# Kernel tuning notes

Hardware: AMD Instinct MI355X
Metric: run time of the kernel (lower is better)

## Reference

```python
import jax, jax.numpy as jnp
import numpy as np

K = 3      # kernel_size
PAD = 1    # (dilation*(K-1)+1)//2 with dilation=1
EPS = 1e-3 # keras BatchNormalization default epsilon


def _unfold(x, k=K, pad=PAD):
    # reflect-pad local-window gather, torch.nn.functional.unfold ordering
    # x: [N,C,H,W] -> [N,C,k*k,H*W]
    N, C, H, W = x.shape
    xp = jnp.pad(x, ((0, 0), (0, 0), (pad, pad), (pad, pad)), mode='reflect')
    pats = jnp.stack([xp[:, :, i:i + H, j:j + W] for i in range(k) for j in range(k)], axis=2)
    return pats.reshape(N, C, k * k, H * W)


def _position(H, W):
    # [1,2,H,W]: channel 0 = x(-1..1 across W), channel 1 = y(-1..1 across H)
    loc_w = jnp.tile(jnp.linspace(-1.0, 1.0, W)[None, :], (H, 1))
    loc_h = jnp.tile(jnp.linspace(-1.0, 1.0, H)[:, None], (1, W))
    return jnp.stack([loc_w, loc_h], axis=0)[None].astype(jnp.float32)


def _bn(x, g, b, m, v):
    # keras BN, default axis=-1 (here the H*W axis), inference mode
    return (x - m) / jnp.sqrt(v + EPS) * g + b


def setup_inputs():
    key = jax.random.key(0)
    ks = jax.random.split(key, 16)
    N, C, H, W = 16, 256, 56, 56
    REL, OUT, SHARE = 16, 64, 8
    HW = H * W
    f = lambda k_, s: jax.random.normal(k_, s, dtype=jnp.float32)
    return {
        'x': f(ks[0], (N, C, H, W)),
        'conv1_w': f(ks[1], (REL, C)) * 0.05,
        'conv2_w': f(ks[2], (REL, C)) * 0.05,
        'conv3_w': f(ks[3], (OUT, C)) * 0.05,
        'convp_w': f(ks[4], (2, 2)),
        'convw1_w': f(ks[5], (REL, REL + 2)) * 0.2,
        'convw2_w': f(ks[6], (OUT // SHARE, REL)) * 0.2,
        'bn1_gamma': 1.0 + 0.1 * f(ks[7], (HW,)),
        'bn1_beta': 0.1 * f(ks[8], (HW,)),
        'bn1_mean': 0.1 * f(ks[9], (HW,)),
        'bn1_var': 1.0 + 0.5 * jax.random.uniform(ks[10], (HW,), dtype=jnp.float32),
        'bn2_gamma': 1.0 + 0.1 * f(ks[11], (HW,)),
        'bn2_beta': 0.1 * f(ks[12], (HW,)),
        'bn2_mean': 0.1 * f(ks[13], (HW,)),
        'bn2_var': 1.0 + 0.5 * jax.random.uniform(ks[14], (HW,), dtype=jnp.float32),
    }


def reference(x, conv1_w, conv2_w, conv3_w, convp_w, convw1_w, convw2_w,
              bn1_gamma, bn1_beta, bn1_mean, bn1_var,
              bn2_gamma, bn2_beta, bn2_mean, bn2_var):
    N, C, H, W = x.shape
    HW = H * W
    # 1x1 convs (channels_first) as channel contractions
    x1 = jnp.einsum('oc,nchw->nohw', conv1_w, x)
    x2 = jnp.einsum('oc,nchw->nohw', conv2_w, x)
    x3 = jnp.einsum('oc,nchw->nohw', conv3_w, x)
    p = jnp.einsum('oc,nchw->nohw', convp_w, _position(H, W))  # [1,2,H,W]
    # subtraction2(x1, x2): center feature minus windowed neighbors -> [N,rel,k^2,HW]
    sub2 = x1.reshape(N, -1, 1, HW) - _unfold(x2)
    # subtraction(p): relative positions -> [1,2,k^2,HW], tiled over batch
    subp = p.reshape(1, 2, 1, HW) - _unfold(p)
    rel = jnp.concatenate([sub2, jnp.tile(subp, (N, 1, 1, 1))], axis=1)  # [N,rel+2,k^2,HW]
    # conv_w: BN -> ReLU -> 1x1 conv -> BN -> ReLU -> 1x1 conv
    h = jax.nn.relu(_bn(rel, bn1_gamma, bn1_beta, bn1_mean, bn1_var))
    h = jnp.einsum('oc,ncjl->nojl', convw1_w, h)
    h = jax.nn.relu(_bn(h, bn2_gamma, bn2_beta, bn2_mean, bn2_var))
    h = jnp.einsum('oc,ncjl->nojl', convw2_w, h)  # [N,out//share,k^2,HW]
    w = jax.nn.softmax(h, axis=-2)                # softmax over the k^2 window axis
    # aggregation: weighted neighbor sum, weight channel shared by share_planes channels
    xu = _unfold(x3)                              # [N,out,k^2,HW]
    c_w = w.shape[1]
    xu = xu.reshape(N, -1, c_w, K * K, HW)        # channel c -> (c//c_w, c%c_w)
    out = jnp.einsum('ncjl,ngcjl->ngcl', w, xu)   # sum over window positions j
    return out.reshape(N, -1, H, W)
```

## Files before the change

kernel.cpp:

```cpp
#include <hip/hip_runtime.h>

typedef short bf16x8 __attribute__((ext_vector_type(8)));
typedef float floatx4 __attribute__((ext_vector_type(4)));
typedef unsigned short ushort4v __attribute__((ext_vector_type(4)));

#define HW 3136
#define NB 16

#define P_CP   0
#define P_W1   4
#define P_W2   292
#define P_FLAG 420
#define P_BN   424
#define PREP_FLOATS (424 + 4 * HW)

#define WS 100

__device__ __forceinline__ unsigned short f2bf(float f) {
    unsigned int u = __float_as_uint(f);
    unsigned int r = (u + 0x7FFFu + ((u >> 16) & 1u)) >> 16;
    return (unsigned short)r;
}
__device__ __forceinline__ float bf2f(unsigned short u) {
    return __uint_as_float(((unsigned int)u) << 16);
}
__device__ __forceinline__ void unp8(uint4 u, float* o) {
    o[0] = bf2f((unsigned short)(u.x & 0xFFFFu)); o[1] = bf2f((unsigned short)(u.x >> 16));
    o[2] = bf2f((unsigned short)(u.y & 0xFFFFu)); o[3] = bf2f((unsigned short)(u.y >> 16));
    o[4] = bf2f((unsigned short)(u.z & 0xFFFFu)); o[5] = bf2f((unsigned short)(u.z >> 16));
    o[6] = bf2f((unsigned short)(u.w & 0xFFFFu)); o[7] = bf2f((unsigned short)(u.w >> 16));
}
__device__ __forceinline__ float ldp(const void* p, int i, int isb) {
    return isb ? bf2f(((const unsigned short*)p)[i]) : ((const float*)p)[i];
}

__device__ __forceinline__ int detect_bf16(const void* varp, int* sflag) {
    if (threadIdx.x == 0) {
        const unsigned short* p = (const unsigned short*)varp;
        int ok = 1;
        for (int i = 0; i < 64; ++i) {
            unsigned short v = p[2 * i];
            if (v < 0x3F80u || v > 0x3FC0u) { ok = 0; break; }
        }
        *sflag = ok;
    }
    __syncthreads();
    return *sflag;
}

struct Stage { unsigned int b[8]; bf16x8 a[2]; };

__device__ __forceinline__ void load_stage(
    int isb, const void* x, size_t xbase, int cb,
    const void* const (&wsA)[2], const int (&roA)[2], int col, Stage& st)
{
    if (isb) {
        const unsigned short* xb = (const unsigned short*)x;
        #pragma unroll
        for (int j = 0; j < 8; ++j)
            st.b[j] = *(const unsigned int*)(xb + xbase + (size_t)(cb + j) * HW);
        #pragma unroll
        for (int rt = 0; rt < 2; ++rt)
            st.a[rt] = *(const bf16x8*)((const unsigned short*)wsA[rt] + (roA[rt] + col) * 256 + cb);
    } else {
        const float* xb = (const float*)x;
        #pragma unroll
        for (int j = 0; j < 8; ++j) {
            float2 f = *(const float2*)(xb + xbase + (size_t)(cb + j) * HW);
            st.b[j] = (unsigned int)f2bf(f.x) | ((unsigned int)f2bf(f.y) << 16);
        }
        #pragma unroll
        for (int rt = 0; rt < 2; ++rt) {
            const float* fp = (const float*)wsA[rt] + (roA[rt] + col) * 256 + cb;
            bf16x8 af;
            #pragma unroll
            for (int j = 0; j < 8; ++j) af[j] = (short)f2bf(fp[j]);
            st.a[rt] = af;
        }
    }
}

__global__ __launch_bounds__(384) void proj_kernel(
    const void* __restrict__ x,
    const void* __restrict__ w1, const void* __restrict__ w2,
    const void* __restrict__ w3,
    const void* __restrict__ cpw, const void* __restrict__ cw1,
    const void* __restrict__ cw2,
    const void* __restrict__ b1g, const void* __restrict__ b1b,
    const void* __restrict__ b1m, const void* __restrict__ b1v,
    const void* __restrict__ b2g, const void* __restrict__ b2b,
    const void* __restrict__ b2m, const void* __restrict__ b2v,
    unsigned short* __restrict__ y,
    float* __restrict__ prep)
{
    __shared__ int sflag;
    const int isb = detect_bf16(b1v, &sflag);
    const int tid = threadIdx.x;

    if (blockIdx.x == 0) {
        for (int i = tid; i < 4;   i += 384) prep[P_CP + i] = ldp(cpw, i, isb);
        for (int i = tid; i < 288; i += 384) prep[P_W1 + i] = ldp(cw1, i, isb);
        for (int i = tid; i < 128; i += 384) prep[P_W2 + i] = ldp(cw2, i, isb);
        if (tid == 0) prep[P_FLAG] = isb ? 1.f : 0.f;
        for (int i = tid; i < HW; i += 384) {
            float a1 = ldp(b1g, i, isb) * rsqrtf(ldp(b1v, i, isb) + 1e-3f);
            float c1 = ldp(b1b, i, isb) - ldp(b1m, i, isb) * a1;
            float a2 = ldp(b2g, i, isb) * rsqrtf(ldp(b2v, i, isb) + 1e-3f);
            float c2 = ldp(b2b, i, isb) - ldp(b2m, i, isb) * a2;
            prep[P_BN + i]          = a1;
            prep[P_BN + HW + i]     = c1;
            prep[P_BN + 2 * HW + i] = a2;
            prep[P_BN + 3 * HW + i] = c2;
        }
    }

    const int blk  = blockIdx.x;
    const int n    = blk / 49;
    const int wave = tid >> 6, lane = tid & 63;
    const int s    = wave & 1;
    const int rg   = wave >> 1;
    const int col  = lane & 15, quad = lane >> 4;
    const int lb   = (blk - n * 49) * 64 + s * 32;
    const int px   = lb + 2 * col;

    const void* wsA[2]; int roA[2];
    if (rg == 0)      { wsA[0] = w1; roA[0] = 0;  wsA[1] = w2; roA[1] = 0;  }
    else if (rg == 1) { wsA[0] = w3; roA[0] = 0;  wsA[1] = w3; roA[1] = 16; }
    else              { wsA[0] = w3; roA[0] = 32; wsA[1] = w3; roA[1] = 48; }

    const size_t xbase = (size_t)n * 256 * HW + px;

    floatx4 acc[2][2];
    const floatx4 z4 = {0.f, 0.f, 0.f, 0.f};
    #pragma unroll
    for (int rt = 0; rt < 2; ++rt)
        #pragma unroll
        for (int t = 0; t < 2; ++t) acc[rt][t] = z4;

    Stage st[2];
    load_stage(isb, x, xbase, quad * 8, wsA, roA, col, st[0]);
    #pragma unroll
    for (int q = 0; q < 8; ++q) {
        if (q < 7)
            load_stage(isb, x, xbase, (q + 1) * 32 + quad * 8, wsA, roA, col, st[(q + 1) & 1]);
        Stage& c = st[q & 1];
        bf16x8 bt0, bt1;
        #pragma unroll
        for (int j = 0; j < 8; ++j) {
            bt0[j] = (short)(c.b[j] & 0xFFFFu);
            bt1[j] = (short)(c.b[j] >> 16);
        }
        #pragma unroll
        for (int rt = 0; rt < 2; ++rt) {
            acc[rt][0] = __builtin_amdgcn_mfma_f32_16x16x32_bf16(c.a[rt], bt0, acc[rt][0], 0, 0, 0);
            acc[rt][1] = __builtin_amdgcn_mfma_f32_16x16x32_bf16(c.a[rt], bt1, acc[rt][1], 0, 0, 0);
        }
    }

    unsigned short* yb = y + ((size_t)n * HW + px) * 96 + rg * 32 + quad * 4;
    #pragma unroll
    for (int rt = 0; rt < 2; ++rt)
        #pragma unroll
        for (int t = 0; t < 2; ++t) {
            ushort4v pk;
            #pragma unroll
            for (int g = 0; g < 4; ++g) pk[g] = f2bf(acc[rt][t][g]);
            *(ushort4v*)(yb + (size_t)t * 96 + rt * 16) = pk;
        }
}

__global__ __launch_bounds__(576) void attn_kernel(
    const unsigned short* __restrict__ yT,
    const float* __restrict__ prep,
    void* __restrict__ out)
{
    __shared__ float wsm[64 * WS];
    const int tid = threadIdx.x;
    const int blk = blockIdx.x;
    const int n   = blk / 49;
    const int l0  = (blk - n * 49) * 64;
    const int isb = prep[P_FLAG] != 0.f;

    {
        const int j = tid >> 6;
        const int p = tid & 63;
        const int l = l0 + p;
        const int h = l / 56, w = l - h * 56;
        const int dy = j / 3 - 1, dx = j - (j / 3) * 3 - 1;
        int hh = h + dy; hh = (hh < 0) ? -hh : ((hh > 55) ? 110 - hh : hh);
        int ww = w + dx; ww = (ww < 0) ? -ww : ((ww > 55) ? 110 - ww : ww);
        const int nbr = hh * 56 + ww;

        const float a1 = prep[P_BN + l];
        const float c1 = prep[P_BN + HW + l];
        const float a2 = prep[P_BN + 2 * HW + l];
        const float c2 = prep[P_BN + 3 * HW + l];

        const unsigned short* y1p = yT + ((size_t)n * HW + l) * 96;
        const unsigned short* y2p = yT + ((size_t)n * HW + nbr) * 96 + 16;
        float y1f[16], y2f[16];
        unp8(*(const uint4*)y1p, y1f);       unp8(*(const uint4*)(y1p + 8), y1f + 8);
        unp8(*(const uint4*)y2p, y2f);       unp8(*(const uint4*)(y2p + 8), y2f + 8);

        float rel[18];
        #pragma unroll
        for (int c = 0; c < 16; ++c)
            rel[c] = fmaxf(fmaf(y1f[c] - y2f[c], a1, c1), 0.f);
        const float dlw = (float)(w - ww) * (2.0f / 55.0f);
        const float dlh = (float)(h - hh) * (2.0f / 55.0f);
        rel[16] = fmaxf(fmaf(prep[P_CP + 0] * dlw + prep[P_CP + 1] * dlh, a1, c1), 0.f);
        rel[17] = fmaxf(fmaf(prep[P_CP + 2] * dlw + prep[P_CP + 3] * dlh, a1, c1), 0.f);

        float h1[16];
        #pragma unroll
        for (int o = 0; o < 16; ++o) {
            float s = 0.f;
            #pragma unroll
            for (int c = 0; c < 18; ++c)
                s = fmaf(prep[P_W1 + o * 18 + c], rel[c], s);
            h1[o] = fmaxf(fmaf(s, a2, c2), 0.f);
        }
        float h2[8];
        #pragma unroll
        for (int o2 = 0; o2 < 8; ++o2) {
            float s = 0.f;
            #pragma unroll
            for (int o = 0; o < 16; ++o)
                s = fmaf(prep[P_W2 + o2 * 16 + o], h1[o], s);
            h2[o2] = s;
        }
        float* wp = &wsm[p * WS + j * 8];
        *(floatx4*)wp       = *(floatx4*)&h2[0];
        *(floatx4*)(wp + 4) = *(floatx4*)&h2[4];
    }
    __syncthreads();

    if (tid < 512) {
        const int c = tid & 7, p = tid >> 3;
        float v[9];
        #pragma unroll
        for (int j = 0; j < 9; ++j) v[j] = wsm[p * WS + j * 8 + c];
        float m = v[0];
        #pragma unroll
        for (int j = 1; j < 9; ++j) m = fmaxf(m, v[j]);
        float s = 0.f;
        #pragma unroll
        for (int j = 0; j < 9; ++j) { v[j] = __expf(v[j] - m); s += v[j]; }
        const float inv = 1.f / s;
        #pragma unroll
        for (int j = 0; j < 9; ++j) wsm[p * WS + j * 8 + c] = v[j] * inv;
    }
    __syncthreads();

    if (tid < 512) {
        const int p  = tid & 63;
        const int k8 = tid >> 6;
        const int l = l0 + p;
        const int h = l / 56, w = l - h * 56;
        int nbr[9];
        #pragma unroll
        for (int dy = 0; dy < 3; ++dy)
            #pragma unroll
            for (int dx = 0; dx < 3; ++dx) {
                int hh = h + dy - 1; hh = (hh < 0) ? -hh : ((hh > 55) ? 110 - hh : hh);
                int ww = w + dx - 1; ww = (ww < 0) ? -ww : ((ww > 55) ? 110 - ww : ww);
                nbr[dy * 3 + dx] = hh * 56 + ww;
            }
        const unsigned short* y3b = yT + (size_t)n * HW * 96 + 32 + k8 * 8;
        float acc8[8];
        #pragma unroll
        for (int k = 0; k < 8; ++k) acc8[k] = 0.f;
        #pragma unroll
        for (int j = 0; j < 9; ++j) {
            uint4 u = *(const uint4*)(y3b + (size_t)nbr[j] * 96);
            float yv[8];
            unp8(u, yv);
            const float* wp = &wsm[p * WS + j * 8];
            float2 w01 = *(const float2*)wp;
            float2 w23 = *(const float2*)(wp + 2);
            float2 w45 = *(const float2*)(wp + 4);
            float2 w67 = *(const float2*)(wp + 6);
            acc8[0] = fmaf(w01.x, yv[0], acc8[0]);
            acc8[1] = fmaf(w01.y, yv[1], acc8[1]);
            acc8[2] = fmaf(w23.x, yv[2], acc8[2]);
            acc8[3] = fmaf(w23.y, yv[3], acc8[3]);
            acc8[4] = fmaf(w45.x, yv[4], acc8[4]);
            acc8[5] = fmaf(w45.y, yv[5], acc8[5]);
            acc8[6] = fmaf(w67.x, yv[6], acc8[6]);
            acc8[7] = fmaf(w67.y, yv[7], acc8[7]);
        }
        const size_t obase = ((size_t)n * 64 + k8 * 8) * HW + l;
        #pragma unroll
        for (int k = 0; k < 8; ++k) {
            if (isb) ((unsigned short*)out)[obase + (size_t)k * HW] = f2bf(acc8[k]);
            else     ((float*)out)[obase + (size_t)k * HW]          = acc8[k];
        }
    }
}

extern "C" void kernel_launch(void* const* d_in, const int* in_sizes, int n_in,
                              void* d_out, int out_size, void* d_ws, size_t ws_size,
                              hipStream_t stream)
{
    const size_t yB = (size_t)NB * HW * 96 * 2;
    unsigned short* y = (unsigned short*)d_ws;
    float* prep = (float*)((char*)d_ws + yB);

    proj_kernel<<<dim3(784), dim3(384), 0, stream>>>(
        d_in[0], d_in[1], d_in[2], d_in[3],
        d_in[4], d_in[5], d_in[6],
        d_in[7], d_in[8], d_in[9], d_in[10],
        d_in[11], d_in[12], d_in[13], d_in[14],
        y, prep);

    attn_kernel<<<dim3(784), dim3(576), 0, stream>>>(y, prep, d_out);
}
```

Measured before the change: 165.6 us.

## Restructure projection GEMM with LDS-staged x tiles and move BN prep into attention kernel

The projection kernel becomes 128-thread blocks over 32 pixels. Each block stages the x tile in LDS using coalesced 16-byte loads, and every wave computes all six 16-row output tiles, so the B operand is reused across w1/w2/w3 instead of being reloaded per row group. It is templated on the input dtype so the branches disappear. The BN folding and the conv weight preparation move out of block 0 of the projection kernel into each attention block, which removes the global prep buffer and the serial work in block 0. The cost is redundant per-block BN and weight loads in the attention kernel, and extra __syncthreads in the projection k-loop.

```diff
diff --git a/kernel.cpp b/kernel.cpp
--- a/kernel.cpp
+++ b/kernel.cpp
@@ -3,17 +3,11 @@
 typedef short bf16x8 __attribute__((ext_vector_type(8)));
 typedef float floatx4 __attribute__((ext_vector_type(4)));
 typedef unsigned short ushort4v __attribute__((ext_vector_type(4)));
+typedef unsigned int uint4v __attribute__((ext_vector_type(4)));
 
 #define HW 3136
 #define NB 16
-
-#define P_CP   0
-#define P_W1   4
-#define P_W2   292
-#define P_FLAG 420
-#define P_BN   424
-#define PREP_FLOATS (424 + 4 * HW)
-
+#define LSTR 35
 #define WS 100
 
 __device__ __forceinline__ unsigned short f2bf(float f) {
@@ -48,138 +42,156 @@
     return *sflag;
 }
 
-struct Stage { unsigned int b[8]; bf16x8 a[2]; };
-
-__device__ __forceinline__ void load_stage(
-    int isb, const void* x, size_t xbase, int cb,
-    const void* const (&wsA)[2], const int (&roA)[2], int col, Stage& st)
-{
-    if (isb) {
-        const unsigned short* xb = (const unsigned short*)x;
-        #pragma unroll
-        for (int j = 0; j < 8; ++j)
-            st.b[j] = *(const unsigned int*)(xb + xbase + (size_t)(cb + j) * HW);
-        #pragma unroll
-        for (int rt = 0; rt < 2; ++rt)
-            st.a[rt] = *(const bf16x8*)((const unsigned short*)wsA[rt] + (roA[rt] + col) * 256 + cb);
+template <int ISB>
+__device__ __forceinline__ void stage_load(const void* x, size_t xrow, int kb,
+                                           int sc2, int spx, unsigned int (&o)[8])
+{
+    if (ISB) {
+        const unsigned short* p = (const unsigned short*)x + xrow + (size_t)(kb + 2 * sc2) * HW + spx;
+        uint4 e = *(const uint4*)p;
+        uint4 d = *(const uint4*)(p + HW);
+        o[0] = (e.x & 0xFFFFu) | (d.x << 16);
+        o[1] = (e.x >> 16)     | (d.x & 0xFFFF0000u);
+        o[2] = (e.y & 0xFFFFu) | (d.y << 16);
+        o[3] = (e.y >> 16)     | (d.y & 0xFFFF0000u);
+        o[4] = (e.z & 0xFFFFu) | (d.z << 16);
+        o[5] = (e.z >> 16)     | (d.z & 0xFFFF0000u);
+        o[6] = (e.w & 0xFFFFu) | (d.w << 16);
+        o[7] = (e.w >> 16)     | (d.w & 0xFFFF0000u);
     } else {
-        const float* xb = (const float*)x;
-        #pragma unroll
-        for (int j = 0; j < 8; ++j) {
-            float2 f = *(const float2*)(xb + xbase + (size_t)(cb + j) * HW);
-            st.b[j] = (unsigned int)f2bf(f.x) | ((unsigned int)f2bf(f.y) << 16);
-        }
-        #pragma unroll
-        for (int rt = 0; rt < 2; ++rt) {
-            const float* fp = (const float*)wsA[rt] + (roA[rt] + col) * 256 + cb;
-            bf16x8 af;
-            #pragma unroll
-            for (int j = 0; j < 8; ++j) af[j] = (short)f2bf(fp[j]);
-            st.a[rt] = af;
-        }
-    }
-}
-
-__global__ __launch_bounds__(384) void proj_kernel(
+        const float* p = (const float*)x + xrow + (size_t)(kb + 2 * sc2) * HW + spx;
+        floatx4 e0 = *(const floatx4*)p,        e1 = *(const floatx4*)(p + 4);
+        floatx4 d0 = *(const floatx4*)(p + HW), d1 = *(const floatx4*)(p + HW + 4);
+        #pragma unroll
+        for (int i = 0; i < 4; ++i) o[i]     = (unsigned int)f2bf(e0[i]) | ((unsigned int)f2bf(d0[i]) << 16);
+        #pragma unroll
+        for (int i = 0; i < 4; ++i) o[4 + i] = (unsigned int)f2bf(e1[i]) | ((unsigned int)f2bf(d1[i]) << 16);
+    }
+}
+
+template <int ISB>
+__device__ __forceinline__ bf16x8 loadA(const void* wp, int row, int cb)
+{
+    if (ISB) return *(const bf16x8*)((const unsigned short*)wp + row * 256 + cb);
+    const float* f = (const float*)wp + row * 256 + cb;
+    bf16x8 a;
+    #pragma unroll
+    for (int j = 0; j < 8; ++j) a[j] = (short)f2bf(f[j]);
+    return a;
+}
+
+template <int ISB>
+__device__ void proj_body(const void* x, const void* w1, const void* w2, const void* w3,
+                          unsigned int* buf, unsigned short* y,
+                          int n, int px0, int wv, int col, int quad, int sc2, int spx)
+{
+    const size_t xrow = (size_t)n * 256 * HW + px0;
+    const void* wp[6] = {w1, w2, w3, w3, w3, w3};
+    const int   ro[6] = {0, 0, 0, 16, 32, 48};
+
+    floatx4 acc[6] = {};
+    unsigned int st[8];
+    stage_load<ISB>(x, xrow, 0, sc2, spx, st);
+    #pragma unroll
+    for (int i = 0; i < 8; ++i) buf[(spx + i) * LSTR + sc2] = st[i];
+
+    bf16x8 Ac[6];
+    #pragma unroll
+    for (int r = 0; r < 6; ++r) Ac[r] = loadA<ISB>(wp[r], ro[r] + col, quad * 8);
+
+    const unsigned int* brow = &buf[(wv * 16 + col) * LSTR];
+
+    #pragma unroll
+    for (int ko = 0; ko < 4; ++ko) {
+        __syncthreads();
+        unsigned int nx[8];
+        if (ko < 3) stage_load<ISB>(x, xrow, 64 * (ko + 1), sc2, spx, nx);
+        #pragma unroll
+        for (int s = 0; s < 2; ++s) {
+            const int ss = ko * 2 + s;
+            const int ib = s * 16 + quad * 4;
+            uint4v bu;
+            bu.x = brow[ib]; bu.y = brow[ib + 1]; bu.z = brow[ib + 2]; bu.w = brow[ib + 3];
+            bf16x8 B = __builtin_bit_cast(bf16x8, bu);
+            bf16x8 An[6];
+            if (ss < 7) {
+                #pragma unroll
+                for (int r = 0; r < 6; ++r)
+                    An[r] = loadA<ISB>(wp[r], ro[r] + col, (ss + 1) * 32 + quad * 8);
+            }
+            #pragma unroll
+            for (int r = 0; r < 6; ++r)
+                acc[r] = __builtin_amdgcn_mfma_f32_16x16x32_bf16(Ac[r], B, acc[r], 0, 0, 0);
+            if (ss < 7) {
+                #pragma unroll
+                for (int r = 0; r < 6; ++r) Ac[r] = An[r];
+            }
+        }
+        __syncthreads();
+        if (ko < 3) {
+            #pragma unroll
+            for (int i = 0; i < 8; ++i) buf[(spx + i) * LSTR + sc2] = nx[i];
+        }
+    }
+
+    unsigned short* yb = y + ((size_t)n * HW + px0 + wv * 16 + col) * 96 + quad * 4;
+    #pragma unroll
+    for (int r = 0; r < 6; ++r) {
+        ushort4v pk;
+        #pragma unroll
+        for (int g = 0; g < 4; ++g) pk[g] = f2bf(acc[r][g]);
+        *(ushort4v*)(yb + r * 16) = pk;
+    }
+}
+
+__global__ __launch_bounds__(128, 4) void proj_kernel(
     const void* __restrict__ x,
     const void* __restrict__ w1, const void* __restrict__ w2,
     const void* __restrict__ w3,
+    const void* __restrict__ b1v,
+    unsigned short* __restrict__ y)
+{
+    __shared__ unsigned int buf[32 * LSTR];
+    __shared__ int sflag;
+    const int isb = detect_bf16(b1v, &sflag);
+
+    const int tid = threadIdx.x;
+    const int gid = blockIdx.x;
+    const int n   = gid / 98;
+    const int pt  = gid - n * 98;
+    const int px0 = pt * 32;
+    const int wv  = tid >> 6, lane = tid & 63;
+    const int col = lane & 15, quad = lane >> 4;
+    const int sc2 = tid >> 2;
+    const int spx = (tid & 3) * 8;
+
+    if (isb) proj_body<1>(x, w1, w2, w3, buf, y, n, px0, wv, col, quad, sc2, spx);
+    else     proj_body<0>(x, w1, w2, w3, buf, y, n, px0, wv, col, quad, sc2, spx);
+}
+
+__global__ __launch_bounds__(576) void attn_kernel(
+    const unsigned short* __restrict__ yT,
     const void* __restrict__ cpw, const void* __restrict__ cw1,
     const void* __restrict__ cw2,
     const void* __restrict__ b1g, const void* __restrict__ b1b,
     const void* __restrict__ b1m, const void* __restrict__ b1v,
     const void* __restrict__ b2g, const void* __restrict__ b2b,
     const void* __restrict__ b2m, const void* __restrict__ b2v,
-    unsigned short* __restrict__ y,
-    float* __restrict__ prep)
-{
+    void* __restrict__ out)
+{
+    __shared__ float wsm[64 * WS];
+    __shared__ float w1f[288], w2f[128], cpf[4];
     __shared__ int sflag;
     const int isb = detect_bf16(b1v, &sflag);
     const int tid = threadIdx.x;
-
-    if (blockIdx.x == 0) {
-        for (int i = tid; i < 4;   i += 384) prep[P_CP + i] = ldp(cpw, i, isb);
-        for (int i = tid; i < 288; i += 384) prep[P_W1 + i] = ldp(cw1, i, isb);
-        for (int i = tid; i < 128; i += 384) prep[P_W2 + i] = ldp(cw2, i, isb);
-        if (tid == 0) prep[P_FLAG] = isb ? 1.f : 0.f;
-        for (int i = tid; i < HW; i += 384) {
-            float a1 = ldp(b1g, i, isb) * rsqrtf(ldp(b1v, i, isb) + 1e-3f);
-            float c1 = ldp(b1b, i, isb) - ldp(b1m, i, isb) * a1;
-            float a2 = ldp(b2g, i, isb) * rsqrtf(ldp(b2v, i, isb) + 1e-3f);
-            float c2 = ldp(b2b, i, isb) - ldp(b2m, i, isb) * a2;
-            prep[P_BN + i]          = a1;
-            prep[P_BN + HW + i]     = c1;
-            prep[P_BN + 2 * HW + i] = a2;
-            prep[P_BN + 3 * HW + i] = c2;
-        }
-    }
-
-    const int blk  = blockIdx.x;
-    const int n    = blk / 49;
-    const int wave = tid >> 6, lane = tid & 63;
-    const int s    = wave & 1;
-    const int rg   = wave >> 1;
-    const int col  = lane & 15, quad = lane >> 4;
-    const int lb   = (blk - n * 49) * 64 + s * 32;
-    const int px   = lb + 2 * col;
-
-    const void* wsA[2]; int roA[2];
-    if (rg == 0)      { wsA[0] = w1; roA[0] = 0;  wsA[1] = w2; roA[1] = 0;  }
-    else if (rg == 1) { wsA[0] = w3; roA[0] = 0;  wsA[1] = w3; roA[1] = 16; }
-    else              { wsA[0] = w3; roA[0] = 32; wsA[1] = w3; roA[1] = 48; }
-
-    const size_t xbase = (size_t)n * 256 * HW + px;
-
-    floatx4 acc[2][2];
-    const floatx4 z4 = {0.f, 0.f, 0.f, 0.f};
-    #pragma unroll
-    for (int rt = 0; rt < 2; ++rt)
-        #pragma unroll
-        for (int t = 0; t < 2; ++t) acc[rt][t] = z4;
-
-    Stage st[2];
-    load_stage(isb, x, xbase, quad * 8, wsA, roA, col, st[0]);
-    #pragma unroll
-    for (int q = 0; q < 8; ++q) {
-        if (q < 7)
-            load_stage(isb, x, xbase, (q + 1) * 32 + quad * 8, wsA, roA, col, st[(q + 1) & 1]);
-        Stage& c = st[q & 1];
-        bf16x8 bt0, bt1;
-        #pragma unroll
-        for (int j = 0; j < 8; ++j) {
-            bt0[j] = (short)(c.b[j] & 0xFFFFu);
-            bt1[j] = (short)(c.b[j] >> 16);
-        }
-        #pragma unroll
-        for (int rt = 0; rt < 2; ++rt) {
-            acc[rt][0] = __builtin_amdgcn_mfma_f32_16x16x32_bf16(c.a[rt], bt0, acc[rt][0], 0, 0, 0);
-            acc[rt][1] = __builtin_amdgcn_mfma_f32_16x16x32_bf16(c.a[rt], bt1, acc[rt][1], 0, 0, 0);
-        }
-    }
-
-    unsigned short* yb = y + ((size_t)n * HW + px) * 96 + rg * 32 + quad * 4;
-    #pragma unroll
-    for (int rt = 0; rt < 2; ++rt)
-        #pragma unroll
-        for (int t = 0; t < 2; ++t) {
-            ushort4v pk;
-            #pragma unroll
-            for (int g = 0; g < 4; ++g) pk[g] = f2bf(acc[rt][t][g]);
-            *(ushort4v*)(yb + (size_t)t * 96 + rt * 16) = pk;
-        }
-}
-
-__global__ __launch_bounds__(576) void attn_kernel(
-    const unsigned short* __restrict__ yT,
-    const float* __restrict__ prep,
-    void* __restrict__ out)
-{
-    __shared__ float wsm[64 * WS];
-    const int tid = threadIdx.x;
+    for (int i = tid; i < 288; i += 576) w1f[i] = ldp(cw1, i, isb);
+    for (int i = tid; i < 128; i += 576) w2f[i] = ldp(cw2, i, isb);
+    if (tid < 4) cpf[tid] = ldp(cpw, tid, isb);
+    __syncthreads();
+
     const int blk = blockIdx.x;
     const int n   = blk / 49;
     const int l0  = (blk - n * 49) * 64;
-    const int isb = prep[P_FLAG] != 0.f;
 
     {
         const int j = tid >> 6;
@@ -191,10 +203,10 @@
         int ww = w + dx; ww = (ww < 0) ? -ww : ((ww > 55) ? 110 - ww : ww);
         const int nbr = hh * 56 + ww;
 
-        const float a1 = prep[P_BN + l];
-        const float c1 = prep[P_BN + HW + l];
-        const float a2 = prep[P_BN + 2 * HW + l];
-        const float c2 = prep[P_BN + 3 * HW + l];
+        const float a1 = ldp(b1g, l, isb) * rsqrtf(ldp(b1v, l, isb) + 1e-3f);
+        const float c1 = ldp(b1b, l, isb) - ldp(b1m, l, isb) * a1;
+        const float a2 = ldp(b2g, l, isb) * rsqrtf(ldp(b2v, l, isb) + 1e-3f);
+        const float c2 = ldp(b2b, l, isb) - ldp(b2m, l, isb) * a2;
 
         const unsigned short* y1p = yT + ((size_t)n * HW + l) * 96;
         const unsigned short* y2p = yT + ((size_t)n * HW + nbr) * 96 + 16;
@@ -208,8 +220,8 @@
             rel[c] = fmaxf(fmaf(y1f[c] - y2f[c], a1, c1), 0.f);
         const float dlw = (float)(w - ww) * (2.0f / 55.0f);
         const float dlh = (float)(h - hh) * (2.0f / 55.0f);
-        rel[16] = fmaxf(fmaf(prep[P_CP + 0] * dlw + prep[P_CP + 1] * dlh, a1, c1), 0.f);
-        rel[17] = fmaxf(fmaf(prep[P_CP + 2] * dlw + prep[P_CP + 3] * dlh, a1, c1), 0.f);
+        rel[16] = fmaxf(fmaf(cpf[0] * dlw + cpf[1] * dlh, a1, c1), 0.f);
+        rel[17] = fmaxf(fmaf(cpf[2] * dlw + cpf[3] * dlh, a1, c1), 0.f);
 
         float h1[16];
         #pragma unroll
@@ -217,7 +229,7 @@
             float s = 0.f;
             #pragma unroll
             for (int c = 0; c < 18; ++c)
-                s = fmaf(prep[P_W1 + o * 18 + c], rel[c], s);
+                s = fmaf(w1f[o * 18 + c], rel[c], s);
             h1[o] = fmaxf(fmaf(s, a2, c2), 0.f);
         }
         float h2[8];
@@ -226,12 +238,12 @@
             float s = 0.f;
             #pragma unroll
             for (int o = 0; o < 16; ++o)
-                s = fmaf(prep[P_W2 + o2 * 16 + o], h1[o], s);
+                s = fmaf(w2f[o2 * 16 + o], h1[o], s);
             h2[o2] = s;
         }
-        float* wp = &wsm[p * WS + j * 8];
-        *(floatx4*)wp       = *(floatx4*)&h2[0];
-        *(floatx4*)(wp + 4) = *(floatx4*)&h2[4];
+        float* wpt = &wsm[p * WS + j * 8];
+        *(floatx4*)wpt       = *(floatx4*)&h2[0];
+        *(floatx4*)(wpt + 4) = *(floatx4*)&h2[4];
     }
     __syncthreads();
 
@@ -275,19 +287,10 @@
             uint4 u = *(const uint4*)(y3b + (size_t)nbr[j] * 96);
             float yv[8];
             unp8(u, yv);
-            const float* wp = &wsm[p * WS + j * 8];
-            float2 w01 = *(const float2*)wp;
-            float2 w23 = *(const float2*)(wp + 2);
-            float2 w45 = *(const float2*)(wp + 4);
-            float2 w67 = *(const float2*)(wp + 6);
-            acc8[0] = fmaf(w01.x, yv[0], acc8[0]);
-            acc8[1] = fmaf(w01.y, yv[1], acc8[1]);
-            acc8[2] = fmaf(w23.x, yv[2], acc8[2]);
-            acc8[3] = fmaf(w23.y, yv[3], acc8[3]);
-            acc8[4] = fmaf(w45.x, yv[4], acc8[4]);
-            acc8[5] = fmaf(w45.y, yv[5], acc8[5]);
-            acc8[6] = fmaf(w67.x, yv[6], acc8[6]);
-            acc8[7] = fmaf(w67.y, yv[7], acc8[7]);
+            const float* wpt = &wsm[p * WS + j * 8];
+            #pragma unroll
+            for (int k = 0; k < 8; ++k)
+                acc8[k] = fmaf(wpt[k], yv[k], acc8[k]);
         }
         const size_t obase = ((size_t)n * 64 + k8 * 8) * HW + l;
         #pragma unroll
@@ -302,16 +305,13 @@
                               void* d_out, int out_size, void* d_ws, size_t ws_size,
                               hipStream_t stream)
 {
-    const size_t yB = (size_t)NB * HW * 96 * 2;
     unsigned short* y = (unsigned short*)d_ws;
-    float* prep = (float*)((char*)d_ws + yB);
-
-    proj_kernel<<<dim3(784), dim3(384), 0, stream>>>(
-        d_in[0], d_in[1], d_in[2], d_in[3],
-        d_in[4], d_in[5], d_in[6],
+
+    proj_kernel<<<dim3(1568), dim3(128), 0, stream>>>(
+        d_in[0], d_in[1], d_in[2], d_in[3], d_in[10], y);
+
+    attn_kernel<<<dim3(784), dim3(576), 0, stream>>>(
+        y, d_in[4], d_in[5], d_in[6],
         d_in[7], d_in[8], d_in[9], d_in[10],
-        d_in[11], d_in[12], d_in[13], d_in[14],
-        y, prep);
-
-    attn_kernel<<<dim3(784), dim3(576), 0, stream>>>(y, prep, d_out);
-}
+        d_in[11], d_in[12], d_in[13], d_in[14], d_out);
+}
```

Result: slower. 192.8 us (+16.5%).

## Retile projection GEMM with wide loads and split y into gather-friendly layouts

Applied to the files above, without the earlier changes.

The projection kernel is reorganised so each 64-lane wave computes one 16-row weight tile over 128 pixels. Each lane loads 8 contiguous pixels per channel with 16-byte vector loads and feeds eight MFMAs per stage, with a template split on the input dtype. The intermediate buffer is split into a compact y1/y2 array (32 channels per pixel) and a y3 array grouped by 8-channel blocks with pixels contiguous. This is meant to make the neighbour gathers in the attention kernel denser and reduce projection load overhead. The cost is that x is re-read by two blocks per pixel tile, the last tile overlaps earlier pixels, and register pressure rises.

```diff
diff --git a/kernel.cpp b/kernel.cpp
--- a/kernel.cpp
+++ b/kernel.cpp
@@ -3,9 +3,10 @@
 typedef short bf16x8 __attribute__((ext_vector_type(8)));
 typedef float floatx4 __attribute__((ext_vector_type(4)));
 typedef unsigned short ushort4v __attribute__((ext_vector_type(4)));
+typedef unsigned int uintx4 __attribute__((ext_vector_type(4)));
 
 #define HW 3136
-#define NB 16
+#define WS 100
 
 #define P_CP   0
 #define P_W1   4
@@ -13,8 +14,6 @@
 #define P_FLAG 420
 #define P_BN   424
 #define PREP_FLOATS (424 + 4 * HW)
-
-#define WS 100
 
 __device__ __forceinline__ unsigned short f2bf(float f) {
     unsigned int u = __float_as_uint(f);
@@ -48,39 +47,73 @@
     return *sflag;
 }
 
-struct Stage { unsigned int b[8]; bf16x8 a[2]; };
-
-__device__ __forceinline__ void load_stage(
-    int isb, const void* x, size_t xbase, int cb,
-    const void* const (&wsA)[2], const int (&roA)[2], int col, Stage& st)
-{
-    if (isb) {
-        const unsigned short* xb = (const unsigned short*)x;
+struct Stage { unsigned int b[32]; bf16x8 a; };
+
+template <int ISB>
+__device__ __forceinline__ void ldstage(const void* x, size_t xb,
+                                        const void* wp, int arow, int ch, Stage& s)
+{
+    if (ISB) {
+        const unsigned short* p = (const unsigned short*)x + xb + (size_t)ch * HW;
         #pragma unroll
         for (int j = 0; j < 8; ++j)
-            st.b[j] = *(const unsigned int*)(xb + xbase + (size_t)(cb + j) * HW);
-        #pragma unroll
-        for (int rt = 0; rt < 2; ++rt)
-            st.a[rt] = *(const bf16x8*)((const unsigned short*)wsA[rt] + (roA[rt] + col) * 256 + cb);
+            *(uint4*)&s.b[4 * j] = *(const uint4*)(p + (size_t)j * HW);
+        s.a = *(const bf16x8*)((const unsigned short*)wp + arow * 256 + ch);
     } else {
-        const float* xb = (const float*)x;
+        const float* p = (const float*)x + xb + (size_t)ch * HW;
         #pragma unroll
         for (int j = 0; j < 8; ++j) {
-            float2 f = *(const float2*)(xb + xbase + (size_t)(cb + j) * HW);
-            st.b[j] = (unsigned int)f2bf(f.x) | ((unsigned int)f2bf(f.y) << 16);
-        }
-        #pragma unroll
-        for (int rt = 0; rt < 2; ++rt) {
-            const float* fp = (const float*)wsA[rt] + (roA[rt] + col) * 256 + cb;
-            bf16x8 af;
-            #pragma unroll
-            for (int j = 0; j < 8; ++j) af[j] = (short)f2bf(fp[j]);
-            st.a[rt] = af;
-        }
-    }
-}
-
-__global__ __launch_bounds__(384) void proj_kernel(
+            floatx4 f0 = *(const floatx4*)(p + (size_t)j * HW);
+            floatx4 f1 = *(const floatx4*)(p + (size_t)j * HW + 4);
+            s.b[4 * j + 0] = (unsigned)f2bf(f0[0]) | ((unsigned)f2bf(f0[1]) << 16);
+            s.b[4 * j + 1] = (unsigned)f2bf(f0[2]) | ((unsigned)f2bf(f0[3]) << 16);
+            s.b[4 * j + 2] = (unsigned)f2bf(f1[0]) | ((unsigned)f2bf(f1[1]) << 16);
+            s.b[4 * j + 3] = (unsigned)f2bf(f1[2]) | ((unsigned)f2bf(f1[3]) << 16);
+        }
+        const float* fp = (const float*)wp + arow * 256 + ch;
+        bf16x8 a;
+        #pragma unroll
+        for (int j = 0; j < 8; ++j) a[j] = (short)f2bf(fp[j]);
+        s.a = a;
+    }
+}
+
+__device__ __forceinline__ void domfma(const Stage& s, floatx4 (&acc)[8])
+{
+    #pragma unroll
+    for (int t = 0; t < 8; ++t) {
+        const int wi = t >> 1;
+        uintx4 uv;
+        #pragma unroll
+        for (int d = 0; d < 4; ++d) {
+            const unsigned lo = s.b[4 * (2 * d) + wi];
+            const unsigned hi = s.b[4 * (2 * d + 1) + wi];
+            const unsigned v = (t & 1) ? ((lo >> 16) | (hi & 0xFFFF0000u))
+                                       : ((lo & 0xFFFFu) | (hi << 16));
+            uv[d] = v;
+        }
+        bf16x8 B = __builtin_bit_cast(bf16x8, uv);
+        acc[t] = __builtin_amdgcn_mfma_f32_16x16x32_bf16(s.a, B, acc[t], 0, 0, 0);
+    }
+}
+
+template <int ISB>
+__device__ void proj_body(const void* x, const void* wp, int arow,
+                          size_t xb, int quad, floatx4 (&acc)[8])
+{
+    Stage s0, s1;
+    ldstage<ISB>(x, xb, wp, arow, quad * 8, s0);
+    #pragma unroll
+    for (int q = 0; q < 8; q += 2) {
+        ldstage<ISB>(x, xb, wp, arow, (q + 1) * 32 + quad * 8, s1);
+        domfma(s0, acc);
+        if (q + 2 < 8)
+            ldstage<ISB>(x, xb, wp, arow, (q + 2) * 32 + quad * 8, s0);
+        domfma(s1, acc);
+    }
+}
+
+__global__ __launch_bounds__(192, 2) void proj_kernel(
     const void* __restrict__ x,
     const void* __restrict__ w1, const void* __restrict__ w2,
     const void* __restrict__ w3,
@@ -90,7 +123,8 @@
     const void* __restrict__ b1m, const void* __restrict__ b1v,
     const void* __restrict__ b2g, const void* __restrict__ b2b,
     const void* __restrict__ b2m, const void* __restrict__ b2v,
-    unsigned short* __restrict__ y,
+    unsigned short* __restrict__ y12,
+    unsigned short* __restrict__ y3a,
     float* __restrict__ prep)
 {
     __shared__ int sflag;
@@ -98,11 +132,11 @@
     const int tid = threadIdx.x;
 
     if (blockIdx.x == 0) {
-        for (int i = tid; i < 4;   i += 384) prep[P_CP + i] = ldp(cpw, i, isb);
-        for (int i = tid; i < 288; i += 384) prep[P_W1 + i] = ldp(cw1, i, isb);
-        for (int i = tid; i < 128; i += 384) prep[P_W2 + i] = ldp(cw2, i, isb);
+        for (int i = tid; i < 4;   i += 192) prep[P_CP + i] = ldp(cpw, i, isb);
+        for (int i = tid; i < 288; i += 192) prep[P_W1 + i] = ldp(cw1, i, isb);
+        for (int i = tid; i < 128; i += 192) prep[P_W2 + i] = ldp(cw2, i, isb);
         if (tid == 0) prep[P_FLAG] = isb ? 1.f : 0.f;
-        for (int i = tid; i < HW; i += 384) {
+        for (int i = tid; i < HW; i += 192) {
             float a1 = ldp(b1g, i, isb) * rsqrtf(ldp(b1v, i, isb) + 1e-3f);
             float c1 = ldp(b1b, i, isb) - ldp(b1m, i, isb) * a1;
             float a2 = ldp(b2g, i, isb) * rsqrtf(ldp(b2v, i, isb) + 1e-3f);
@@ -114,63 +148,47 @@
         }
     }
 
-    const int blk  = blockIdx.x;
-    const int n    = blk / 49;
-    const int wave = tid >> 6, lane = tid & 63;
-    const int s    = wave & 1;
-    const int rg   = wave >> 1;
-    const int col  = lane & 15, quad = lane >> 4;
-    const int lb   = (blk - n * 49) * 64 + s * 32;
-    const int px   = lb + 2 * col;
-
-    const void* wsA[2]; int roA[2];
-    if (rg == 0)      { wsA[0] = w1; roA[0] = 0;  wsA[1] = w2; roA[1] = 0;  }
-    else if (rg == 1) { wsA[0] = w3; roA[0] = 0;  wsA[1] = w3; roA[1] = 16; }
-    else              { wsA[0] = w3; roA[0] = 32; wsA[1] = w3; roA[1] = 48; }
-
-    const size_t xbase = (size_t)n * 256 * HW + px;
-
-    floatx4 acc[2][2];
-    const floatx4 z4 = {0.f, 0.f, 0.f, 0.f};
+    const int b   = blockIdx.x;
+    const int n   = b / 50, r = b - n * 50;
+    const int rh  = r / 25, pt = r - rh * 25;
+    const int px0 = (pt < 24) ? pt * 128 : 3008;
+    const int wv  = tid >> 6, lane = tid & 63;
+    const int col = lane & 15, quad = lane >> 4;
+    const int rt  = rh * 3 + wv;
+
+    const void* wp; int ro;
+    if      (rt == 0) { wp = w1; ro = 0;  }
+    else if (rt == 1) { wp = w2; ro = 0;  }
+    else if (rt == 2) { wp = w3; ro = 0;  }
+    else if (rt == 3) { wp = w3; ro = 16; }
+    else if (rt == 4) { wp = w3; ro = 32; }
+    else              { wp = w3; ro = 48; }
+
+    const size_t xb = (size_t)n * 256 * HW + px0 + 8 * col;
+
+    floatx4 acc[8] = {};
+    if (isb) proj_body<1>(x, wp, ro + col, xb, quad, acc);
+    else     proj_body<0>(x, wp, ro + col, xb, quad, acc);
+
+    const int chq = quad * 4;
     #pragma unroll
-    for (int rt = 0; rt < 2; ++rt)
-        #pragma unroll
-        for (int t = 0; t < 2; ++t) acc[rt][t] = z4;
-
-    Stage st[2];
-    load_stage(isb, x, xbase, quad * 8, wsA, roA, col, st[0]);
-    #pragma unroll
-    for (int q = 0; q < 8; ++q) {
-        if (q < 7)
-            load_stage(isb, x, xbase, (q + 1) * 32 + quad * 8, wsA, roA, col, st[(q + 1) & 1]);
-        Stage& c = st[q & 1];
-        bf16x8 bt0, bt1;
-        #pragma unroll
-        for (int j = 0; j < 8; ++j) {
-            bt0[j] = (short)(c.b[j] & 0xFFFFu);
-            bt1[j] = (short)(c.b[j] >> 16);
-        }
-        #pragma unroll
-        for (int rt = 0; rt < 2; ++rt) {
-            acc[rt][0] = __builtin_amdgcn_mfma_f32_16x16x32_bf16(c.a[rt], bt0, acc[rt][0], 0, 0, 0);
-            acc[rt][1] = __builtin_amdgcn_mfma_f32_16x16x32_bf16(c.a[rt], bt1, acc[rt][1], 0, 0, 0);
-        }
-    }
-
-    unsigned short* yb = y + ((size_t)n * HW + px) * 96 + rg * 32 + quad * 4;
-    #pragma unroll
-    for (int rt = 0; rt < 2; ++rt)
-        #pragma unroll
-        for (int t = 0; t < 2; ++t) {
-            ushort4v pk;
-            #pragma unroll
-            for (int g = 0; g < 4; ++g) pk[g] = f2bf(acc[rt][t][g]);
-            *(ushort4v*)(yb + (size_t)t * 96 + rt * 16) = pk;
-        }
+    for (int t = 0; t < 8; ++t) {
+        const int px = px0 + 8 * col + t;
+        ushort4v pk;
+        #pragma unroll
+        for (int g = 0; g < 4; ++g) pk[g] = f2bf(acc[t][g]);
+        if (rt < 2) {
+            *(ushort4v*)(y12 + ((size_t)n * HW + px) * 32 + rt * 16 + chq) = pk;
+        } else {
+            const int k8 = 2 * (rt - 2) + (quad >> 1);
+            *(ushort4v*)(y3a + (((size_t)n * 8 + k8) * HW + px) * 8 + (quad & 1) * 4) = pk;
+        }
+    }
 }
 
 __global__ __launch_bounds__(576) void attn_kernel(
-    const unsigned short* __restrict__ yT,
+    const unsigned short* __restrict__ y12,
+    const unsigned short* __restrict__ y3a,
     const float* __restrict__ prep,
     void* __restrict__ out)
 {
@@ -196,8 +214,8 @@
         const float a2 = prep[P_BN + 2 * HW + l];
         const float c2 = prep[P_BN + 3 * HW + l];
 
-        const unsigned short* y1p = yT + ((size_t)n * HW + l) * 96;
-        const unsigned short* y2p = yT + ((size_t)n * HW + nbr) * 96 + 16;
+        const unsigned short* y1p = y12 + ((size_t)n * HW + l) * 32;
+        const unsigned short* y2p = y12 + ((size_t)n * HW + nbr) * 32 + 16;
         float y1f[16], y2f[16];
         unp8(*(const uint4*)y1p, y1f);       unp8(*(const uint4*)(y1p + 8), y1f + 8);
         unp8(*(const uint4*)y2p, y2f);       unp8(*(const uint4*)(y2p + 8), y2f + 8);
@@ -229,9 +247,9 @@
                 s = fmaf(prep[P_W2 + o2 * 16 + o], h1[o], s);
             h2[o2] = s;
         }
-        float* wp = &wsm[p * WS + j * 8];
-        *(floatx4*)wp       = *(floatx4*)&h2[0];
-        *(floatx4*)(wp + 4) = *(floatx4*)&h2[4];
+        float* wpt = &wsm[p * WS + j * 8];
+        *(floatx4*)wpt       = *(floatx4*)&h2[0];
+        *(floatx4*)(wpt + 4) = *(floatx4*)&h2[4];
     }
     __syncthreads();
 
@@ -266,28 +284,19 @@
                 int ww = w + dx - 1; ww = (ww < 0) ? -ww : ((ww > 55) ? 110 - ww : ww);
                 nbr[dy * 3 + dx] = hh * 56 + ww;
             }
-        const unsigned short* y3b = yT + (size_t)n * HW * 96 + 32 + k8 * 8;
+        const unsigned short* y3b = y3a + ((size_t)n * 8 + k8) * HW * 8;
         float acc8[8];
         #pragma unroll
         for (int k = 0; k < 8; ++k) acc8[k] = 0.f;
         #pragma unroll
         for (int j = 0; j < 9; ++j) {
-            uint4 u = *(const uint4*)(y3b + (size_t)nbr[j] * 96);
+            uint4 u = *(const uint4*)(y3b + (size_t)nbr[j] * 8);
             float yv[8];
             unp8(u, yv);
-            const float* wp = &wsm[p * WS + j * 8];
-            float2 w01 = *(const float2*)wp;
-            float2 w23 = *(const float2*)(wp + 2);
-            float2 w45 = *(const float2*)(wp + 4);
-            float2 w67 = *(const float2*)(wp + 6);
-            acc8[0] = fmaf(w01.x, yv[0], acc8[0]);
-            acc8[1] = fmaf(w01.y, yv[1], acc8[1]);
-            acc8[2] = fmaf(w23.x, yv[2], acc8[2]);
-            acc8[3] = fmaf(w23.y, yv[3], acc8[3]);
-            acc8[4] = fmaf(w45.x, yv[4], acc8[4]);
-            acc8[5] = fmaf(w45.y, yv[5], acc8[5]);
-            acc8[6] = fmaf(w67.x, yv[6], acc8[6]);
-            acc8[7] = fmaf(w67.y, yv[7], acc8[7]);
+            const float* wpt = &wsm[p * WS + j * 8];
+            #pragma unroll
+            for (int k = 0; k < 8; ++k)
+                acc8[k] = fmaf(wpt[k], yv[k], acc8[k]);
         }
         const size_t obase = ((size_t)n * 64 + k8 * 8) * HW + l;
         #pragma unroll
@@ -302,16 +311,19 @@
                               void* d_out, int out_size, void* d_ws, size_t ws_size,
                               hipStream_t stream)
 {
-    const size_t yB = (size_t)NB * HW * 96 * 2;
-    unsigned short* y = (unsigned short*)d_ws;
-    float* prep = (float*)((char*)d_ws + yB);
-
-    proj_kernel<<<dim3(784), dim3(384), 0, stream>>>(
+    const size_t y12B = (size_t)16 * HW * 32 * 2;
+    const size_t y3aB = (size_t)16 * 8 * HW * 8 * 2;
+
+    unsigned short* y12 = (unsigned short*)d_ws;
+    unsigned short* y3a = (unsigned short*)((char*)d_ws + y12B);
+    float* prep = (float*)((char*)d_ws + y12B + y3aB);
+
+    proj_kernel<<<dim3(800), dim3(192), 0, stream>>>(
         d_in[0], d_in[1], d_in[2], d_in[3],
         d_in[4], d_in[5], d_in[6],
         d_in[7], d_in[8], d_in[9], d_in[10],
         d_in[11], d_in[12], d_in[13], d_in[14],
-        y, prep);
-
-    attn_kernel<<<dim3(784), dim3(576), 0, stream>>>(y, prep, d_out);
-}
+        y12, y3a, prep);
+
+    attn_kernel<<<dim3(784), dim3(576), 0, stream>>>(y12, y3a, prep, d_out);
+}
```

Result: faster. 155.9 us (-5.8%).
